# Performance work log

Hardware: AMD Instinct MI355X
Metric: run time of the kernel (lower is better)

Reference implementation:

```python
import jax, jax.numpy as jnp
import numpy as np

N = 50257   # vocab size
D = 128     # embedding_dim
B = 2048    # batch
C = 10      # context window size


def setup_inputs() -> dict:
    key = jax.random.key(0)
    ks = jax.random.split(key, 16)
    s = 0.02
    return {
        "x_batch": jax.random.randint(ks[0], (B,), 0, N),
        "context_words_batch": jax.random.randint(ks[1], (B, C), 0, N),
        "eps": jax.random.normal(ks[2], (B, D), dtype=jnp.float32),
        # learned parameters
        "inf_emb": jax.random.normal(ks[3], (N, D), dtype=jnp.float32) * s,
        "W_aff": jax.random.normal(ks[4], (D, 2 * D), dtype=jnp.float32) * s,
        "b_aff": jnp.zeros((D,), dtype=jnp.float32),
        "W_mu": jax.random.normal(ks[5], (D, D), dtype=jnp.float32) * s,
        "b_mu": jnp.zeros((D,), dtype=jnp.float32),
        "W_sig": jax.random.normal(ks[6], (D, D), dtype=jnp.float32) * s,
        "b_sig": jnp.zeros((D,), dtype=jnp.float32),
        "gen_sigma_emb": jax.random.normal(ks[7], (N, D), dtype=jnp.float32) * s,
        "W_gen": jax.random.normal(ks[8], (N, D), dtype=jnp.float32) * s,
        "b_gen": jnp.zeros((N,), dtype=jnp.float32),
    }


def reference(x_batch, context_words_batch, eps, inf_emb, W_aff, b_aff,
              W_mu, b_mu, W_sig, b_sig, gen_sigma_emb, W_gen, b_gen):
    # ---- inference network (vectorized over batch and context) ----
    center = inf_emb[x_batch]                    # [B, D]
    ctx = inf_emb[context_words_batch]           # [B, C, D]
    center_rep = jnp.broadcast_to(center[:, None, :], ctx.shape)  # [B, C, D]
    cat = jnp.concatenate([center_rep, ctx], axis=-1)             # [B, C, 2D]
    h = jax.nn.relu(jnp.einsum("bce,de->bcd", cat, W_aff) + b_aff)
    h_sum = h.sum(axis=1)                        # [B, D]
    inf_mu = h_sum @ W_mu.T + b_mu               # [B, D]
    inf_sigma = jax.nn.softplus(h_sum @ W_sig.T + b_sig)

    # ---- reparameterized sample ----
    z = inf_mu + eps * inf_sigma                 # [B, D]

    # ---- generative / reconstruction term ----
    logits = z @ W_gen.T + b_gen                 # [B, N] (dominant intermediate)
    logp = jax.nn.log_softmax(logits, axis=-1)
    recon = jnp.take_along_axis(logp, context_words_batch, axis=1).sum(-1)  # [B]

    # ---- KL term (faithful to original, incl. use of generative sigma) ----
    sigma = jax.nn.softplus(gen_sigma_emb[x_batch])  # [B, D]
    kl = (jnp.log(sigma / inf_sigma)
          + (inf_sigma ** 2 + (inf_mu - sigma) ** 2) / (2.0 * sigma ** 2)
          - 0.5).sum(-1)                        # [B]

    return (kl - recon).mean()
```

## Files before the change

### kernel.cpp

```cpp
#include <hip/hip_runtime.h>
#include <float.h>
#include <math.h>

#define NV 50257
#define D 128
#define B 2048
#define C 10

#define NVPAD 50272
#define NTILES (NVPAD / 16)
#define NSTREAM 128
#define NG4 (NVPAD * D / 4)
#define LOG2E 1.44269504088896f
#define SC1 0x7F7F7F7F

typedef __attribute__((ext_vector_type(8))) short short8;
typedef __attribute__((ext_vector_type(8))) int int8v;
typedef __attribute__((ext_vector_type(4))) float float4v;

__device__ __forceinline__ float softplus_f(float x) {
    return fmaxf(x, 0.f) + log1pf(expf(-fabsf(x)));
}

__device__ __forceinline__ short f2bf(float f) {
    unsigned u = __float_as_uint(f);
    unsigned r = (u + 0x7FFFu + ((u >> 16) & 1u)) >> 16;
    return (short)r;
}

__global__ __launch_bounds__(256) void k_convert(
    const float* __restrict__ wg, const float* __restrict__ waff,
    const float* __restrict__ wmu, const float* __restrict__ wsig,
    const float* __restrict__ b_gen,
    unsigned char* __restrict__ w8_o, short* __restrict__ waff_o,
    short* __restrict__ wmu_o, short* __restrict__ wsig_o,
    float* __restrict__ bg2, float* __restrict__ out)
{
    const int i4 = blockIdx.x * 256 + threadIdx.x;
    if (i4 == 0) out[0] = 0.f;
    if (i4 < NG4) {
        const int e0 = i4 * 4;
        int pk = 0;
        if (e0 < NV * D) {
            const float4 g = ((const float4*)wg)[i4];
            pk = __builtin_amdgcn_cvt_pk_fp8_f32(g.x, g.y, 0, false);
            pk = __builtin_amdgcn_cvt_pk_fp8_f32(g.z, g.w, pk, true);
        }
        ((int*)w8_o)[i4] = pk;
        return;
    }
    const int j = i4 - NG4;
    if (j < 16384) {
        const float4* src; short4* dst; int jj;
        if (j < 8192)       { src = (const float4*)waff; dst = (short4*)waff_o; jj = j; }
        else if (j < 12288) { src = (const float4*)wmu;  dst = (short4*)wmu_o;  jj = j - 8192; }
        else                { src = (const float4*)wsig; dst = (short4*)wsig_o; jj = j - 12288; }
        const float4 g = src[jj];
        short4 o;
        o.x = f2bf(g.x); o.y = f2bf(g.y); o.z = f2bf(g.z); o.w = f2bf(g.w);
        dst[jj] = o;
    } else {
        const int jj = j - 16384;
        if (jj < NVPAD / 4) {
            const int e0 = jj * 4;
            float4 o;
            o.x = (e0 + 0 < NV) ? b_gen[e0 + 0] * LOG2E : -INFINITY;
            o.y = (e0 + 1 < NV) ? b_gen[e0 + 1] * LOG2E : -INFINITY;
            o.z = (e0 + 2 < NV) ? b_gen[e0 + 2] * LOG2E : -INFINITY;
            o.w = (e0 + 3 < NV) ? b_gen[e0 + 3] * LOG2E : -INFINITY;
            ((float4*)bg2)[jj] = o;
        }
    }
}

__global__ __launch_bounds__(512) void k_infer(
    const int* __restrict__ x_batch, const int* __restrict__ ctxw,
    const float* __restrict__ eps, const float* __restrict__ inf_emb,
    const short* __restrict__ waff_bf, const float* __restrict__ b_aff,
    const short* __restrict__ wmu_bf, const float* __restrict__ b_mu,
    const short* __restrict__ wsig_bf, const float* __restrict__ b_sig,
    const float* __restrict__ gen_sig_emb,
    float* __restrict__ z_out, unsigned char* __restrict__ z8_out,
    float* __restrict__ kl_out)
{
    const int b0 = blockIdx.x * 16;
    const int t = threadIdx.x;
    const int wv = t >> 6;
    const int lane = t & 63;
    const int col16 = lane & 15;
    const int quad = lane >> 4;

    __shared__ float hsp[8][16][132];
    __shared__ float kl_s[8][16];

    const int brow = b0 + col16;
    const int cidx = x_batch[brow];

    short8 ce[4];
    #pragma unroll
    for (int ks = 0; ks < 4; ++ks) {
        const float* p = inf_emb + (size_t)cidx * D + ks * 32 + quad * 8;
        const float4 g0 = *(const float4*)p;
        const float4 g1 = *(const float4*)(p + 4);
        short8 v;
        v[0] = f2bf(g0.x); v[1] = f2bf(g0.y); v[2] = f2bf(g0.z); v[3] = f2bf(g0.w);
        v[4] = f2bf(g1.x); v[5] = f2bf(g1.y); v[6] = f2bf(g1.z); v[7] = f2bf(g1.w);
        ce[ks] = v;
    }

    float4v U[8];
    #pragma unroll
    for (int dt = 0; dt < 8; ++dt) {
        float4v acc = {0.f, 0.f, 0.f, 0.f};
        #pragma unroll
        for (int ks = 0; ks < 4; ++ks) {
            const short8 bw = *(const short8*)(waff_bf + (dt * 16 + col16) * 256 + ks * 32 + quad * 8);
            acc = __builtin_amdgcn_mfma_f32_16x16x32_bf16(ce[ks], bw, acc, 0, 0, 0);
        }
        U[dt] = acc;
    }
    float ba[8];
    #pragma unroll
    for (int dt = 0; dt < 8; ++dt) ba[dt] = b_aff[dt * 16 + col16];

    float4v H[8];
    #pragma unroll
    for (int dt = 0; dt < 8; ++dt) H[dt] = (float4v){0.f, 0.f, 0.f, 0.f};

    const int nctx = (wv < 2) ? 2 : 1;
    for (int cc = 0; cc < nctx; ++cc) {
        const int c = wv + cc * 8;
        const int widx = ctxw[brow * C + c];
        short8 cx[4];
        #pragma unroll
        for (int ks = 0; ks < 4; ++ks) {
            const float* p = inf_emb + (size_t)widx * D + ks * 32 + quad * 8;
            const float4 g0 = *(const float4*)p;
            const float4 g1 = *(const float4*)(p + 4);
            short8 v;
            v[0] = f2bf(g0.x); v[1] = f2bf(g0.y); v[2] = f2bf(g0.z); v[3] = f2bf(g0.w);
            v[4] = f2bf(g1.x); v[5] = f2bf(g1.y); v[6] = f2bf(g1.z); v[7] = f2bf(g1.w);
            cx[ks] = v;
        }
        #pragma unroll
        for (int dt = 0; dt < 8; ++dt) {
            float4v a = {0.f, 0.f, 0.f, 0.f};
            #pragma unroll
            for (int ks = 0; ks < 4; ++ks) {
                const short8 bw = *(const short8*)(waff_bf + (dt * 16 + col16) * 256 + 128 + ks * 32 + quad * 8);
                a = __builtin_amdgcn_mfma_f32_16x16x32_bf16(cx[ks], bw, a, 0, 0, 0);
            }
            #pragma unroll
            for (int r = 0; r < 4; ++r)
                H[dt][r] += fmaxf(U[dt][r] + a[r] + ba[dt], 0.f);
        }
    }

    #pragma unroll
    for (int dt = 0; dt < 8; ++dt)
        #pragma unroll
        for (int r = 0; r < 4; ++r)
            hsp[wv][quad * 4 + r][dt * 16 + col16] = H[dt][r];
    __syncthreads();

    short8 ha[4];
    #pragma unroll
    for (int ks = 0; ks < 4; ++ks) {
        const int off = ks * 32 + quad * 8;
        float4 s0 = {0.f, 0.f, 0.f, 0.f}, s1 = {0.f, 0.f, 0.f, 0.f};
        #pragma unroll
        for (int w = 0; w < 8; ++w) {
            const float4 a0 = *(const float4*)&hsp[w][col16][off];
            const float4 a1 = *(const float4*)&hsp[w][col16][off + 4];
            s0.x += a0.x; s0.y += a0.y; s0.z += a0.z; s0.w += a0.w;
            s1.x += a1.x; s1.y += a1.y; s1.z += a1.z; s1.w += a1.w;
        }
        short8 v;
        v[0] = f2bf(s0.x); v[1] = f2bf(s0.y); v[2] = f2bf(s0.z); v[3] = f2bf(s0.w);
        v[4] = f2bf(s1.x); v[5] = f2bf(s1.y); v[6] = f2bf(s1.z); v[7] = f2bf(s1.w);
        ha[ks] = v;
    }

    int xb2[4];
    #pragma unroll
    for (int r = 0; r < 4; ++r) xb2[r] = x_batch[b0 + quad * 4 + r];

    float klp[4] = {0.f, 0.f, 0.f, 0.f};
    {
        const int nt = wv;
        float4v mu4 = {0.f, 0.f, 0.f, 0.f};
        float4v sg4 = {0.f, 0.f, 0.f, 0.f};
        #pragma unroll
        for (int ks = 0; ks < 4; ++ks) {
            const short8 bm = *(const short8*)(wmu_bf + (nt * 16 + col16) * 128 + ks * 32 + quad * 8);
            const short8 bs = *(const short8*)(wsig_bf + (nt * 16 + col16) * 128 + ks * 32 + quad * 8);
            mu4 = __builtin_amdgcn_mfma_f32_16x16x32_bf16(ha[ks], bm, mu4, 0, 0, 0);
            sg4 = __builtin_amdgcn_mfma_f32_16x16x32_bf16(ha[ks], bs, sg4, 0, 0, 0);
        }
        const int d = nt * 16 + col16;
        const float bmu = b_mu[d];
        const float bsg = b_sig[d];
        #pragma unroll
        for (int r = 0; r < 4; ++r) {
            const int b = b0 + quad * 4 + r;
            const float mu = mu4[r] + bmu;
            const float sg = sg4[r] + bsg;
            const float isig = softplus_f(sg);
            const float e = eps[b * D + d];
            const float zz = fmaf(e, isig, mu);
            z_out[b * D + d] = zz;
            const int pk = __builtin_amdgcn_cvt_pk_fp8_f32(zz * LOG2E, 0.f, 0, false);
            z8_out[b * D + d] = (unsigned char)(pk & 0xFF);
            const float gs = softplus_f(gen_sig_emb[(size_t)xb2[r] * D + d]);
            const float diff = mu - gs;
            klp[r] += logf(gs / isig) + (isig * isig + diff * diff) / (2.f * gs * gs) - 0.5f;
        }
    }
    #pragma unroll
    for (int off = 1; off < 16; off <<= 1)
        #pragma unroll
        for (int r = 0; r < 4; ++r)
            klp[r] += __shfl_xor(klp[r], off, 64);
    if (col16 == 0) {
        #pragma unroll
        for (int r = 0; r < 4; ++r)
            kl_s[wv][quad * 4 + r] = klp[r];
    }
    __syncthreads();
    if (t < 16) {
        float s = 0.f;
        #pragma unroll
        for (int w = 0; w < 8; ++w) s += kl_s[w][t];
        kl_out[b0 + t] = s;
    }
}

#define LOADT8(bf, g, T) { \
    const int v_ = (T) < NTILES; \
    const int tt_ = v_ ? (T) : 0; \
    bf = *(const int8v*)(w8 + (size_t)(tt_ * 16 + col16) * D + quad * 32); \
    g = v_ ? bg2t[tt_ * 16 + col16] : -INFINITY; }

#define COMP8(bf, g) { \
    _Pragma("unroll") \
    for (int rt = 0; rt < 4; ++rt) { \
        float4v c = {g, g, g, g}; \
        c = __builtin_amdgcn_mfma_scale_f32_16x16x128_f8f6f4( \
                afrag[rt], bf, c, 0, 0, 0, SC1, 0, SC1); \
        _Pragma("unroll") \
        for (int r = 0; r < 4; ++r) \
            sums[rt][r] += __builtin_amdgcn_exp2f(c[r]); \
    } }

__global__ __launch_bounds__(256) void k_lse_mfma(
    const unsigned char* __restrict__ z8, const unsigned char* __restrict__ w8,
    const float* __restrict__ bg2t, float* __restrict__ part_s)
{
    const int bid = blockIdx.x;
    const int s = bid & 127;
    const int x = bid >> 7;
    const int t = threadIdx.x;
    const int wv = t >> 6;
    const int lane = t & 63;
    const int col16 = lane & 15;
    const int quad = lane >> 4;
    const int rowbase = x * 256 + wv * 64;

    int8v afrag[4];
    #pragma unroll
    for (int rt = 0; rt < 4; ++rt)
        afrag[rt] = *(const int8v*)(z8 + (size_t)(rowbase + rt * 16 + col16) * D + quad * 32);

    float sums[4][4];
    #pragma unroll
    for (int rt = 0; rt < 4; ++rt)
        #pragma unroll
        for (int r = 0; r < 4; ++r) sums[rt][r] = 0.f;

    int8v bA, bB, bC, bD;
    float gA, gB, gC, gD;
    LOADT8(bA, gA, s);
    LOADT8(bB, gB, s + 128);
    LOADT8(bC, gC, s + 256);
    LOADT8(bD, gD, s + 384);
    #pragma unroll 1
    for (int j = 0; j < 24; j += 4) {
        COMP8(bA, gA); LOADT8(bA, gA, s + (j + 4) * 128);
        COMP8(bB, gB); LOADT8(bB, gB, s + (j + 5) * 128);
        COMP8(bC, gC); LOADT8(bC, gC, s + (j + 6) * 128);
        COMP8(bD, gD); LOADT8(bD, gD, s + (j + 7) * 128);
    }
    COMP8(bA, gA); COMP8(bB, gB); COMP8(bC, gC); COMP8(bD, gD);

    #pragma unroll
    for (int off = 1; off < 16; off <<= 1)
        #pragma unroll
        for (int rt = 0; rt < 4; ++rt)
            #pragma unroll
            for (int r = 0; r < 4; ++r)
                sums[rt][r] += __shfl_xor(sums[rt][r], off, 64);

    if (col16 == 0) {
        #pragma unroll
        for (int rt = 0; rt < 4; ++rt)
            #pragma unroll
            for (int r = 0; r < 4; ++r) {
                const int row = rowbase + rt * 16 + quad * 4 + r;
                part_s[row * NSTREAM + s] = sums[rt][r];
            }
    }
}

__global__ __launch_bounds__(256) void k_final(
    const float* __restrict__ z, const float* __restrict__ W_gen,
    const float* __restrict__ b_gen, const int* __restrict__ ctxw,
    const float* __restrict__ part_s, const float* __restrict__ kl,
    float* __restrict__ out)
{
    const int t = threadIdx.x;
    const int wv = t >> 6;
    const int lane = t & 63;
    __shared__ float red[4];

    float wsum = 0.f;
    #pragma unroll
    for (int rr = 0; rr < 2; ++rr) {
        const int b = blockIdx.x * 8 + wv * 2 + rr;

        int idxs[C];
        #pragma unroll
        for (int c = 0; c < C; ++c) idxs[c] = ctxw[b * C + c];
        float2 wv2[C];
        #pragma unroll
        for (int c = 0; c < C; ++c)
            wv2[c] = *(const float2*)(W_gen + (size_t)idxs[c] * D + lane * 2);
        float sum_bg = 0.f;
        #pragma unroll
        for (int c = 0; c < C; ++c) sum_bg += b_gen[idxs[c]];

        float sv = part_s[b * NSTREAM + lane] + part_s[b * NSTREAM + 64 + lane];
        const float z0 = z[b * D + lane * 2];
        const float z1 = z[b * D + lane * 2 + 1];

        float acc = 0.f;
        #pragma unroll
        for (int c = 0; c < C; ++c) {
            acc = fmaf(z0, wv2[c].x, acc);
            acc = fmaf(z1, wv2[c].y, acc);
        }
        #pragma unroll
        for (int off = 32; off > 0; off >>= 1) {
            sv  += __shfl_xor(sv, off, 64);
            acc += __shfl_xor(acc, off, 64);
        }
        if (lane == 0) {
            const float lse = logf(sv);
            const float recon = acc + sum_bg - C * lse;
            wsum += kl[b] - recon;
        }
    }
    if (lane == 0) red[wv] = wsum;
    __syncthreads();
    if (t == 0) atomicAdd(out, (red[0] + red[1] + red[2] + red[3]) * (1.f / B));
}

extern "C" void kernel_launch(void* const* d_in, const int* in_sizes, int n_in,
                              void* d_out, int out_size, void* d_ws, size_t ws_size,
                              hipStream_t stream) {
    const int* x_batch = (const int*)d_in[0];
    const int* ctxw    = (const int*)d_in[1];
    const float* eps   = (const float*)d_in[2];
    const float* inf_emb = (const float*)d_in[3];
    const float* W_aff = (const float*)d_in[4];
    const float* b_aff = (const float*)d_in[5];
    const float* W_mu  = (const float*)d_in[6];
    const float* b_mu  = (const float*)d_in[7];
    const float* W_sig = (const float*)d_in[8];
    const float* b_sig = (const float*)d_in[9];
    const float* gen_sig = (const float*)d_in[10];
    const float* W_gen = (const float*)d_in[11];
    const float* b_gen = (const float*)d_in[12];
    float* out = (float*)d_out;

    char* ws = (char*)d_ws;
    float* z      = (float*)ws;   ws += (size_t)B * D * 4;
    float* part_s = (float*)ws;   ws += (size_t)B * NSTREAM * 4;
    float* kl     = (float*)ws;   ws += (size_t)B * 4;
    float* bg2    = (float*)ws;   ws += (size_t)NVPAD * 4;
    unsigned char* z8 = (unsigned char*)ws;  ws += (size_t)B * D;
    unsigned char* w8 = (unsigned char*)ws;  ws += (size_t)NVPAD * D;
    short* waff_bf = (short*)ws;  ws += (size_t)128 * 256 * 2;
    short* wmu_bf  = (short*)ws;  ws += (size_t)128 * 128 * 2;
    short* wsig_bf = (short*)ws;  ws += (size_t)128 * 128 * 2;

    const int conv_items = NG4 + 16384 + NVPAD / 4;
    hipLaunchKernelGGL(k_convert, dim3((conv_items + 255) / 256), dim3(256), 0, stream,
                       W_gen, W_aff, W_mu, W_sig, b_gen,
                       w8, waff_bf, wmu_bf, wsig_bf, bg2, out);
    hipLaunchKernelGGL(k_infer, dim3(B / 16), dim3(512), 0, stream,
                       x_batch, ctxw, eps, inf_emb, waff_bf, b_aff, wmu_bf, b_mu,
                       wsig_bf, b_sig, gen_sig, z, z8, kl);
    hipLaunchKernelGGL(k_lse_mfma, dim3(8 * NSTREAM), dim3(256), 0, stream,
                       z8, w8, bg2, part_s);
    hipLaunchKernelGGL(k_final, dim3(B / 8), dim3(256), 0, stream,
                       z, W_gen, b_gen, ctxw, part_s, kl, out);
}
```

Measured before the change: 190.4 us.

## Fuse W_gen FP8 conversion into inference kernel and parallelize context over ten waves

```diff
diff --git a/kernel.cpp b/kernel.cpp
--- a/kernel.cpp
+++ b/kernel.cpp
@@ -28,28 +28,14 @@
     return (short)r;
 }
 
-__global__ __launch_bounds__(256) void k_convert(
-    const float* __restrict__ wg, const float* __restrict__ waff,
-    const float* __restrict__ wmu, const float* __restrict__ wsig,
-    const float* __restrict__ b_gen,
-    unsigned char* __restrict__ w8_o, short* __restrict__ waff_o,
-    short* __restrict__ wmu_o, short* __restrict__ wsig_o,
-    float* __restrict__ bg2, float* __restrict__ out)
+__global__ __launch_bounds__(256) void k_pre(
+    const float* __restrict__ waff, const float* __restrict__ wmu,
+    const float* __restrict__ wsig, const float* __restrict__ b_gen,
+    short* __restrict__ waff_o, short* __restrict__ wmu_o,
+    short* __restrict__ wsig_o, float* __restrict__ bg2, float* __restrict__ out)
 {
-    const int i4 = blockIdx.x * 256 + threadIdx.x;
-    if (i4 == 0) out[0] = 0.f;
-    if (i4 < NG4) {
-        const int e0 = i4 * 4;
-        int pk = 0;
-        if (e0 < NV * D) {
-            const float4 g = ((const float4*)wg)[i4];
-            pk = __builtin_amdgcn_cvt_pk_fp8_f32(g.x, g.y, 0, false);
-            pk = __builtin_amdgcn_cvt_pk_fp8_f32(g.z, g.w, pk, true);
-        }
-        ((int*)w8_o)[i4] = pk;
-        return;
-    }
-    const int j = i4 - NG4;
+    const int j = blockIdx.x * 256 + threadIdx.x;
+    if (j == 0) out[0] = 0.f;
     if (j < 16384) {
         const float4* src; short4* dst; int jj;
         if (j < 8192)       { src = (const float4*)waff; dst = (short4*)waff_o; jj = j; }
@@ -73,120 +59,132 @@
     }
 }
 
-__global__ __launch_bounds__(512) void k_infer(
+#define CONVB 629
+__global__ __launch_bounds__(640) void k_main(
     const int* __restrict__ x_batch, const int* __restrict__ ctxw,
     const float* __restrict__ eps, const float* __restrict__ inf_emb,
     const short* __restrict__ waff_bf, const float* __restrict__ b_aff,
     const short* __restrict__ wmu_bf, const float* __restrict__ b_mu,
     const short* __restrict__ wsig_bf, const float* __restrict__ b_sig,
-    const float* __restrict__ gen_sig_emb,
+    const float* __restrict__ gen_sig_emb, const float* __restrict__ wg,
+    unsigned char* __restrict__ w8,
     float* __restrict__ z_out, unsigned char* __restrict__ z8_out,
     float* __restrict__ kl_out)
 {
-    const int b0 = blockIdx.x * 16;
+    const int bid = blockIdx.x;
     const int t = threadIdx.x;
+
+    __shared__ float us[16][132];
+    __shared__ float hsp[10][16][132];
+    __shared__ float kl_s[8][16];
+
+    if (bid >= 128) {
+        const int base = (bid - 128) * (640 * 4) + t;
+        #pragma unroll
+        for (int k = 0; k < 4; ++k) {
+            const int i4 = base + k * 640;
+            if (i4 < NG4) {
+                const int e0 = i4 * 4;
+                int pk = 0;
+                if (e0 < NV * D) {
+                    const float4 g = ((const float4*)wg)[i4];
+                    pk = __builtin_amdgcn_cvt_pk_fp8_f32(g.x, g.y, 0, false);
+                    pk = __builtin_amdgcn_cvt_pk_fp8_f32(g.z, g.w, pk, true);
+                }
+                ((int*)w8)[i4] = pk;
+            }
+        }
+        return;
+    }
+
+    const int b0 = bid * 16;
     const int wv = t >> 6;
     const int lane = t & 63;
     const int col16 = lane & 15;
     const int quad = lane >> 4;
-
-    __shared__ float hsp[8][16][132];
-    __shared__ float kl_s[8][16];
-
     const int brow = b0 + col16;
-    const int cidx = x_batch[brow];
-
-    short8 ce[4];
+
+    const int widx = ctxw[brow * C + wv];
+    short8 cx[4];
     #pragma unroll
     for (int ks = 0; ks < 4; ++ks) {
-        const float* p = inf_emb + (size_t)cidx * D + ks * 32 + quad * 8;
+        const float* p = inf_emb + (size_t)widx * D + ks * 32 + quad * 8;
         const float4 g0 = *(const float4*)p;
         const float4 g1 = *(const float4*)(p + 4);
         short8 v;
         v[0] = f2bf(g0.x); v[1] = f2bf(g0.y); v[2] = f2bf(g0.z); v[3] = f2bf(g0.w);
         v[4] = f2bf(g1.x); v[5] = f2bf(g1.y); v[6] = f2bf(g1.z); v[7] = f2bf(g1.w);
-        ce[ks] = v;
-    }
-
-    float4v U[8];
-    #pragma unroll
-    for (int dt = 0; dt < 8; ++dt) {
-        float4v acc = {0.f, 0.f, 0.f, 0.f};
+        cx[ks] = v;
+    }
+
+    if (wv < 8) {
+        const int cidx = x_batch[brow];
+        short8 ce[4];
         #pragma unroll
         for (int ks = 0; ks < 4; ++ks) {
-            const short8 bw = *(const short8*)(waff_bf + (dt * 16 + col16) * 256 + ks * 32 + quad * 8);
-            acc = __builtin_amdgcn_mfma_f32_16x16x32_bf16(ce[ks], bw, acc, 0, 0, 0);
-        }
-        U[dt] = acc;
-    }
-    float ba[8];
-    #pragma unroll
-    for (int dt = 0; dt < 8; ++dt) ba[dt] = b_aff[dt * 16 + col16];
-
-    float4v H[8];
-    #pragma unroll
-    for (int dt = 0; dt < 8; ++dt) H[dt] = (float4v){0.f, 0.f, 0.f, 0.f};
-
-    const int nctx = (wv < 2) ? 2 : 1;
-    for (int cc = 0; cc < nctx; ++cc) {
-        const int c = wv + cc * 8;
-        const int widx = ctxw[brow * C + c];
-        short8 cx[4];
-        #pragma unroll
-        for (int ks = 0; ks < 4; ++ks) {
-            const float* p = inf_emb + (size_t)widx * D + ks * 32 + quad * 8;
+            const float* p = inf_emb + (size_t)cidx * D + ks * 32 + quad * 8;
             const float4 g0 = *(const float4*)p;
             const float4 g1 = *(const float4*)(p + 4);
             short8 v;
             v[0] = f2bf(g0.x); v[1] = f2bf(g0.y); v[2] = f2bf(g0.z); v[3] = f2bf(g0.w);
             v[4] = f2bf(g1.x); v[5] = f2bf(g1.y); v[6] = f2bf(g1.z); v[7] = f2bf(g1.w);
-            cx[ks] = v;
-        }
-        #pragma unroll
-        for (int dt = 0; dt < 8; ++dt) {
-            float4v a = {0.f, 0.f, 0.f, 0.f};
+            ce[ks] = v;
+        }
+        float4v acc = {0.f, 0.f, 0.f, 0.f};
+        #pragma unroll
+        for (int ks = 0; ks < 4; ++ks) {
+            const short8 bw = *(const short8*)(waff_bf + (wv * 16 + col16) * 256 + ks * 32 + quad * 8);
+            acc = __builtin_amdgcn_mfma_f32_16x16x32_bf16(ce[ks], bw, acc, 0, 0, 0);
+        }
+        #pragma unroll
+        for (int r = 0; r < 4; ++r)
+            us[quad * 4 + r][wv * 16 + col16] = acc[r];
+    }
+    __syncthreads();
+
+    float ba[8];
+    #pragma unroll
+    for (int dt = 0; dt < 8; ++dt) ba[dt] = b_aff[dt * 16 + col16];
+
+    #pragma unroll
+    for (int dt = 0; dt < 8; ++dt) {
+        float4v a = {0.f, 0.f, 0.f, 0.f};
+        #pragma unroll
+        for (int ks = 0; ks < 4; ++ks) {
+            const short8 bw = *(const short8*)(waff_bf + (dt * 16 + col16) * 256 + 128 + ks * 32 + quad * 8);
+            a = __builtin_amdgcn_mfma_f32_16x16x32_bf16(cx[ks], bw, a, 0, 0, 0);
+        }
+        #pragma unroll
+        for (int r = 0; r < 4; ++r) {
+            const float u = us[quad * 4 + r][dt * 16 + col16];
+            hsp[wv][quad * 4 + r][dt * 16 + col16] = fmaxf(u + a[r] + ba[dt], 0.f);
+        }
+    }
+    __syncthreads();
+
+    if (wv < 8) {
+        short8 ha[4];
+        #pragma unroll
+        for (int ks = 0; ks < 4; ++ks) {
+            const int off = ks * 32 + quad * 8;
+            float4 s0 = {0.f, 0.f, 0.f, 0.f}, s1 = {0.f, 0.f, 0.f, 0.f};
             #pragma unroll
-            for (int ks = 0; ks < 4; ++ks) {
-                const short8 bw = *(const short8*)(waff_bf + (dt * 16 + col16) * 256 + 128 + ks * 32 + quad * 8);
-                a = __builtin_amdgcn_mfma_f32_16x16x32_bf16(cx[ks], bw, a, 0, 0, 0);
+            for (int w = 0; w < 10; ++w) {
+                const float4 a0 = *(const float4*)&hsp[w][col16][off];
+                const float4 a1 = *(const float4*)&hsp[w][col16][off + 4];
+                s0.x += a0.x; s0.y += a0.y; s0.z += a0.z; s0.w += a0.w;
+                s1.x += a1.x; s1.y += a1.y; s1.z += a1.z; s1.w += a1.w;
             }
-            #pragma unroll
-            for (int r = 0; r < 4; ++r)
-                H[dt][r] += fmaxf(U[dt][r] + a[r] + ba[dt], 0.f);
-        }
-    }
-
-    #pragma unroll
-    for (int dt = 0; dt < 8; ++dt)
-        #pragma unroll
-        for (int r = 0; r < 4; ++r)
-            hsp[wv][quad * 4 + r][dt * 16 + col16] = H[dt][r];
-    __syncthreads();
-
-    short8 ha[4];
-    #pragma unroll
-    for (int ks = 0; ks < 4; ++ks) {
-        const int off = ks * 32 + quad * 8;
-        float4 s0 = {0.f, 0.f, 0.f, 0.f}, s1 = {0.f, 0.f, 0.f, 0.f};
-        #pragma unroll
-        for (int w = 0; w < 8; ++w) {
-            const float4 a0 = *(const float4*)&hsp[w][col16][off];
-            const float4 a1 = *(const float4*)&hsp[w][col16][off + 4];
-            s0.x += a0.x; s0.y += a0.y; s0.z += a0.z; s0.w += a0.w;
-            s1.x += a1.x; s1.y += a1.y; s1.z += a1.z; s1.w += a1.w;
-        }
-        short8 v;
-        v[0] = f2bf(s0.x); v[1] = f2bf(s0.y); v[2] = f2bf(s0.z); v[3] = f2bf(s0.w);
-        v[4] = f2bf(s1.x); v[5] = f2bf(s1.y); v[6] = f2bf(s1.z); v[7] = f2bf(s1.w);
-        ha[ks] = v;
-    }
-
-    int xb2[4];
-    #pragma unroll
-    for (int r = 0; r < 4; ++r) xb2[r] = x_batch[b0 + quad * 4 + r];
-
-    float klp[4] = {0.f, 0.f, 0.f, 0.f};
-    {
+            short8 v;
+            v[0] = f2bf(s0.x); v[1] = f2bf(s0.y); v[2] = f2bf(s0.z); v[3] = f2bf(s0.w);
+            v[4] = f2bf(s1.x); v[5] = f2bf(s1.y); v[6] = f2bf(s1.z); v[7] = f2bf(s1.w);
+            ha[ks] = v;
+        }
+
+        int xb2[4];
+        #pragma unroll
+        for (int r = 0; r < 4; ++r) xb2[r] = x_batch[b0 + quad * 4 + r];
+
         const int nt = wv;
         float4v mu4 = {0.f, 0.f, 0.f, 0.f};
         float4v sg4 = {0.f, 0.f, 0.f, 0.f};
@@ -200,6 +198,7 @@
         const int d = nt * 16 + col16;
         const float bmu = b_mu[d];
         const float bsg = b_sig[d];
+        float klp[4];
         #pragma unroll
         for (int r = 0; r < 4; ++r) {
             const int b = b0 + quad * 4 + r;
@@ -213,18 +212,18 @@
             z8_out[b * D + d] = (unsigned char)(pk & 0xFF);
             const float gs = softplus_f(gen_sig_emb[(size_t)xb2[r] * D + d]);
             const float diff = mu - gs;
-            klp[r] += logf(gs / isig) + (isig * isig + diff * diff) / (2.f * gs * gs) - 0.5f;
-        }
-    }
-    #pragma unroll
-    for (int off = 1; off < 16; off <<= 1)
-        #pragma unroll
-        for (int r = 0; r < 4; ++r)
-            klp[r] += __shfl_xor(klp[r], off, 64);
-    if (col16 == 0) {
-        #pragma unroll
-        for (int r = 0; r < 4; ++r)
-            kl_s[wv][quad * 4 + r] = klp[r];
+            klp[r] = logf(gs / isig) + (isig * isig + diff * diff) / (2.f * gs * gs) - 0.5f;
+        }
+        #pragma unroll
+        for (int off = 1; off < 16; off <<= 1)
+            #pragma unroll
+            for (int r = 0; r < 4; ++r)
+                klp[r] += __shfl_xor(klp[r], off, 64);
+        if (col16 == 0) {
+            #pragma unroll
+            for (int r = 0; r < 4; ++r)
+                kl_s[wv][quad * 4 + r] = klp[r];
+        }
     }
     __syncthreads();
     if (t < 16) {
@@ -393,13 +392,13 @@
     short* wmu_bf  = (short*)ws;  ws += (size_t)128 * 128 * 2;
     short* wsig_bf = (short*)ws;  ws += (size_t)128 * 128 * 2;
 
-    const int conv_items = NG4 + 16384 + NVPAD / 4;
-    hipLaunchKernelGGL(k_convert, dim3((conv_items + 255) / 256), dim3(256), 0, stream,
-                       W_gen, W_aff, W_mu, W_sig, b_gen,
-                       w8, waff_bf, wmu_bf, wsig_bf, bg2, out);
-    hipLaunchKernelGGL(k_infer, dim3(B / 16), dim3(512), 0, stream,
+    const int pre_items = 16384 + NVPAD / 4;
+    hipLaunchKernelGGL(k_pre, dim3((pre_items + 255) / 256), dim3(256), 0, stream,
+                       W_aff, W_mu, W_sig, b_gen,
+                       waff_bf, wmu_bf, wsig_bf, bg2, out);
+    hipLaunchKernelGGL(k_main, dim3(128 + CONVB), dim3(640), 0, stream,
                        x_batch, ctxw, eps, inf_emb, waff_bf, b_aff, wmu_bf, b_mu,
-                       wsig_bf, b_sig, gen_sig, z, z8, kl);
+                       wsig_bf, b_sig, gen_sig, W_gen, w8, z, z8, kl);
     hipLaunchKernelGGL(k_lse_mfma, dim3(8 * NSTREAM), dim3(256), 0, stream,
                        z8, w8, bg2, part_s);
     hipLaunchKernelGGL(k_final, dim3(B / 8), dim3(256), 0, stream,
```

New measurement: 183.5 us. 1.04x faster.
